# Performance work log

Measured on AMD Instinct MI355X. Metric: run time of the kernel, lower is better.

## Reference

```python
import jax, jax.numpy as jnp
import numpy as np

B, S, H, E, V = 64, 96, 1024, 512, 32000
START_TOKEN = 1


def setup_inputs() -> dict:
    key = jax.random.key(0)
    ks = jax.random.split(key, 12)
    sc = 0.02
    return {
        "encoder_outputs": jax.random.normal(ks[0], (B, S, H), jnp.float32),
        "encoder_hidden": jax.random.normal(ks[1], (1, B, H), jnp.float32),
        "emb_table": jax.random.normal(ks[2], (V, E), jnp.float32) * sc,
        "Wa": jax.random.normal(ks[3], (H, H), jnp.float32) * sc,
        "Ua": jax.random.normal(ks[4], (H, H), jnp.float32) * sc,
        "Va": jax.random.normal(ks[5], (H,), jnp.float32) * sc,
        "W_ih": jax.random.normal(ks[6], (3 * H, E + H), jnp.float32) * sc,
        "W_hh": jax.random.normal(ks[7], (3 * H, H), jnp.float32) * sc,
        "b_ih": jax.random.normal(ks[8], (3 * H,), jnp.float32) * sc,
        "b_hh": jax.random.normal(ks[9], (3 * H,), jnp.float32) * sc,
        "W_out": jax.random.normal(ks[10], (V, H), jnp.float32) * sc,
        "b_out": jax.random.normal(ks[11], (V,), jnp.float32) * sc,
        "max_length": 32,
    }


def _decode(encoder_outputs, encoder_hidden, emb_table, Wa, Ua, Va,
            W_ih, W_hh, b_ih, b_hh, W_out, b_out, max_length):
    keys = encoder_outputs                       # [B,S,H]
    keys_Ua = jnp.einsum('bsh,gh->bsg', keys, Ua)  # Ua(keys), hoisted (same math every step)
    h0 = encoder_hidden[0]                       # [B,H], num_layers==1
    tok0 = jnp.full((keys.shape[0],), START_TOKEN, dtype=jnp.int32)

    def step(carry, _):
        h, tok = carry
        emb = jax.nn.relu(emb_table[tok])                        # [B,E]
        # Bahdanau scores: Va(tanh(Wa(q)) + Ua(keys))  (tanh only on Wa(q), as in source)
        q = jnp.tanh(h @ Wa.T)                                   # [B,H]
        scores = jnp.einsum('bsh,h->bs', q[:, None, :] + keys_Ua, Va)  # [B,S]
        w = jax.nn.softmax(scores, axis=-1)                      # [B,S]
        ctx = jnp.einsum('bs,bsh->bh', w, keys)                  # [B,H]
        x = jnp.concatenate([emb, ctx], axis=-1)                 # [B,E+H]
        # GRU cell (torch gate order: r, z, n)
        gi = x @ W_ih.T + b_ih                                   # [B,3H]
        gh = h @ W_hh.T + b_hh
        Hd = h.shape[-1]
        r = jax.nn.sigmoid(gi[:, :Hd] + gh[:, :Hd])
        z = jax.nn.sigmoid(gi[:, Hd:2 * Hd] + gh[:, Hd:2 * Hd])
        n = jnp.tanh(gi[:, 2 * Hd:] + r * gh[:, 2 * Hd:])
        h_new = (1.0 - z) * n + z * h
        logits = h_new @ W_out.T + b_out                         # [B,V]
        tok_new = jnp.argmax(logits, axis=-1).astype(jnp.int32)  # greedy (no teacher forcing)
        return (h_new, tok_new), (logits, w)

    (h_T, _), (logits_seq, attn_seq) = jax.lax.scan(step, (h0, tok0), None, length=max_length)
    decoder_outputs = jnp.transpose(logits_seq, (1, 0, 2))  # [B,T,V]
    attentions = jnp.transpose(attn_seq, (1, 0, 2))         # [B,T,S]
    return decoder_outputs, h_T[None], attentions


def reference(encoder_outputs, encoder_hidden, emb_table, Wa, Ua, Va,
              W_ih, W_hh, b_ih, b_hh, W_out, b_out, max_length):
    return _decode(encoder_outputs, encoder_hidden, emb_table, Wa, Ua, Va,
                   W_ih, W_hh, b_ih, b_hh, W_out, b_out, max_length)
```

## Files before the change

kernel.cpp:

```cpp
#include <hip/hip_runtime.h>
#include <hip/hip_bf16.h>

#define Bdim 64
#define Sdim 96
#define Hdim 1024
#define Edim 512
#define Vdim 32000
#define Tdim 32
#define O1 65536000L
#define O2 65601536L
#define TV 1024000L

typedef short short8 __attribute__((ext_vector_type(8)));
typedef float f32x4 __attribute__((ext_vector_type(4)));

__device__ __forceinline__ unsigned short f2bf(float f) {
  unsigned u = __builtin_bit_cast(unsigned, f);
  unsigned r = (u + 0x7fffu + ((u >> 16) & 1u)) >> 16;
  return (unsigned short)r;
}


__global__ void k_u1(const float* __restrict__ Va, const float* __restrict__ Ua,
                     float* __restrict__ pu) {
  int gc = blockIdx.x & 15, hc = blockIdx.x >> 4;
  int lane = threadIdx.x & 63, wv = threadIdx.x >> 6;
  int g = gc * 64 + lane;
  int h0 = hc * 128 + wv * 32;
  float acc = 0.f;
  #pragma unroll 8
  for (int h = h0; h < h0 + 32; ++h) acc = fmaf(Va[h], Ua[(long)h * Hdim + g], acc);
  __shared__ float red[4][64];
  red[wv][lane] = acc;
  __syncthreads();
  if (threadIdx.x < 64)
    pu[hc * Hdim + gc * 64 + threadIdx.x] =
        red[0][threadIdx.x] + red[1][threadIdx.x] + red[2][threadIdx.x] + red[3][threadIdx.x];
}

__global__ void k_u2(const float* __restrict__ pu, float* __restrict__ u) {
  int g = blockIdx.x * 256 + threadIdx.x;
  float s = 0.f;
  #pragma unroll
  for (int i = 0; i < 8; ++i) s += pu[i * Hdim + g];
  u[g] = s;
}

__global__ void k_sc(const float* __restrict__ keys, const float* __restrict__ u,
                     float* __restrict__ sc) {
  int wid = blockIdx.x * 4 + (threadIdx.x >> 6);
  int lane = threadIdx.x & 63;
  int b = wid / Sdim, s = wid % Sdim;
  const float* kp = keys + ((long)b * Sdim + s) * Hdim;
  float acc = 0.f;
  #pragma unroll 4
  for (int g = lane; g < Hdim; g += 64) acc = fmaf(kp[g], u[g], acc);
  for (int off = 32; off; off >>= 1) acc += __shfl_down(acc, off);
  if (lane == 0) sc[wid] = acc;
}

__global__ void k_softmax(const float* __restrict__ sc, float* __restrict__ wbuf,
                          float* __restrict__ attn) {
  int b = blockIdx.x, tid = threadIdx.x;
  __shared__ float sv[128];
  __shared__ float sw[Sdim];
  float v = (tid < Sdim) ? sc[b * Sdim + tid] : -1e30f;
  sv[tid] = v;
  __syncthreads();
  for (int off = 64; off >= 1; off >>= 1) {
    if (tid < off) sv[tid] = fmaxf(sv[tid], sv[tid + off]);
    __syncthreads();
  }
  float mx = sv[0];
  __syncthreads();
  float e = (tid < Sdim) ? expf(v - mx) : 0.f;
  sv[tid] = e;
  __syncthreads();
  for (int off = 64; off >= 1; off >>= 1) {
    if (tid < off) sv[tid] += sv[tid + off];
    __syncthreads();
  }
  float sm = sv[0];
  if (tid < Sdim) {
    float w = e / sm;
    sw[tid] = w;
    wbuf[b * Sdim + tid] = w;
  }
  __syncthreads();
  for (int i = tid; i < Tdim * Sdim; i += 128)
    attn[(long)b * (Tdim * Sdim) + i] = sw[i % Sdim];
}

__global__ void k_ctx(const float* __restrict__ wbuf, const float* __restrict__ keys,
                      float* __restrict__ ctxT) {
  int b = blockIdx.x >> 3, slab = blockIdx.x & 7;
  int tid = threadIdx.x;
  __shared__ float sw[Sdim];
  __shared__ float4 red[8][32];
  if (tid < Sdim) sw[tid] = wbuf[b * Sdim + tid];
  __syncthreads();
  int hq = tid & 31, sg = tid >> 5;
  const float* kp = keys + ((long)b * Sdim + sg * 12) * Hdim + slab * 128 + hq * 4;
  float4 acc = {0.f, 0.f, 0.f, 0.f};
  #pragma unroll
  for (int s = 0; s < 12; ++s) {
    float4 k4 = *(const float4*)(kp + (long)s * Hdim);
    float w = sw[sg * 12 + s];
    acc.x = fmaf(w, k4.x, acc.x); acc.y = fmaf(w, k4.y, acc.y);
    acc.z = fmaf(w, k4.z, acc.z); acc.w = fmaf(w, k4.w, acc.w);
  }
  red[sg][hq] = acc;
  __syncthreads();
  if (tid < 128) {
    int hq2 = tid >> 2, c = tid & 3;
    float s = 0.f;
    #pragma unroll
    for (int i = 0; i < 8; ++i) s += ((const float*)&red[i][hq2])[c];
    ctxT[(slab * 128 + hq2 * 4 + c) * 64 + b] = s;
  }
}

__global__ void k_gctx(const float* __restrict__ ctxT, const float* __restrict__ Wih,
                       const float* __restrict__ bih, float* __restrict__ gctxT) {
  int j = blockIdx.x;
  int lane = threadIdx.x & 63, wv = threadIdx.x >> 6;
  const float* wp = Wih + (long)j * 1536 + Edim + wv * 256;
  const float* xp = ctxT + (wv * 256) * 64 + lane;
  float acc = 0.f;
  #pragma unroll 8
  for (int h = 0; h < 256; ++h) acc = fmaf(xp[h * 64], wp[h], acc);
  __shared__ float red[4][64];
  red[wv][lane] = acc;
  __syncthreads();
  if (threadIdx.x < 64)
    gctxT[(long)j * 64 + threadIdx.x] = red[0][threadIdx.x] + red[1][threadIdx.x] +
                                        red[2][threadIdx.x] + red[3][threadIdx.x] + bih[j];
}

__global__ void k_init(const float* __restrict__ h0, const float* __restrict__ embt,
                       float* __restrict__ hT, float* __restrict__ embT) {
  int idx = blockIdx.x * 256 + threadIdx.x;
  if (idx < Bdim * Hdim) {
    int b = idx >> 10, k = idx & 1023;
    hT[k * 64 + b] = h0[idx];
  } else {
    int j = idx - Bdim * Hdim;
    if (j < Edim * 64) {
      int e = j >> 6;
      float x = embt[1 * Edim + e];
      embT[j] = x > 0.f ? x : 0.f;
    }
  }
}

__global__ void k_w2b(const float* __restrict__ W, unsigned short* __restrict__ Wb) {
  long i = ((long)blockIdx.x * 256 + threadIdx.x) * 8;
  float4 a = *(const float4*)(W + i);
  float4 b = *(const float4*)(W + i + 4);
  short8 v;
  v[0] = (short)f2bf(a.x); v[1] = (short)f2bf(a.y); v[2] = (short)f2bf(a.z); v[3] = (short)f2bf(a.w);
  v[4] = (short)f2bf(b.x); v[5] = (short)f2bf(b.y); v[6] = (short)f2bf(b.z); v[7] = (short)f2bf(b.w);
  *(short8*)(Wb + i) = v;
}


__launch_bounds__(512)
__global__ void k_gru(const float* __restrict__ hT_in, float* __restrict__ hT_out,
                      const float* __restrict__ embT, const float* __restrict__ gctxT,
                      const float* __restrict__ Wih, const float* __restrict__ Whh,
                      const float* __restrict__ bhh,
                      float* __restrict__ hrow, unsigned short* __restrict__ hb) {
  __shared__ float wE[6][Edim];
  __shared__ float wH[6][Hdim];
  __shared__ float red[8][12][64];
  int tid = threadIdx.x, lane = tid & 63, wv = tid >> 6;
  int hid0 = blockIdx.x * 2;
  for (int i = tid; i < 6 * 128; i += 512) {
    int r = i >> 7, c = (i & 127) << 2;
    int row = (r >> 1) * Hdim + hid0 + (r & 1);
    *(float4*)&wE[r][c] = *(const float4*)(Wih + (long)row * 1536 + c);
  }
  for (int i = tid; i < 6 * 256; i += 512) {
    int r = i >> 8, c = (i & 255) << 2;
    int row = (r >> 1) * Hdim + hid0 + (r & 1);
    *(float4*)&wH[r][c] = *(const float4*)(Whh + (long)row * Hdim + c);
  }
  __syncthreads();
  float aE[6] = {0, 0, 0, 0, 0, 0}, aH[6] = {0, 0, 0, 0, 0, 0};
  int e0 = wv * 64;
  #pragma unroll 2
  for (int e = e0; e < e0 + 64; e += 4) {
    float x0 = embT[(e + 0) * 64 + lane];
    float x1 = embT[(e + 1) * 64 + lane];
    float x2 = embT[(e + 2) * 64 + lane];
    float x3 = embT[(e + 3) * 64 + lane];
    #pragma unroll
    for (int r = 0; r < 6; ++r) {
      float4 w = *(const float4*)&wE[r][e];
      aE[r] = fmaf(w.x, x0, aE[r]); aE[r] = fmaf(w.y, x1, aE[r]);
      aE[r] = fmaf(w.z, x2, aE[r]); aE[r] = fmaf(w.w, x3, aE[r]);
    }
  }
  int k0 = wv * 128;
  #pragma unroll 2
  for (int k = k0; k < k0 + 128; k += 4) {
    float x0 = hT_in[(k + 0) * 64 + lane];
    float x1 = hT_in[(k + 1) * 64 + lane];
    float x2 = hT_in[(k + 2) * 64 + lane];
    float x3 = hT_in[(k + 3) * 64 + lane];
    #pragma unroll
    for (int r = 0; r < 6; ++r) {
      float4 w = *(const float4*)&wH[r][k];
      aH[r] = fmaf(w.x, x0, aH[r]); aH[r] = fmaf(w.y, x1, aH[r]);
      aH[r] = fmaf(w.z, x2, aH[r]); aH[r] = fmaf(w.w, x3, aH[r]);
    }
  }
  #pragma unroll
  for (int r = 0; r < 6; ++r) {
    red[wv][r][lane] = aE[r];
    red[wv][6 + r][lane] = aH[r];
  }
  __syncthreads();
  if (tid < 128) {
    int hi = tid >> 6, b = tid & 63, hid = hid0 + hi;
    float sE[3] = {0, 0, 0}, sH[3] = {0, 0, 0};
    #pragma unroll
    for (int w2 = 0; w2 < 8; ++w2) {
      #pragma unroll
      for (int q = 0; q < 3; ++q) {
        sE[q] += red[w2][q * 2 + hi][b];
        sH[q] += red[w2][6 + q * 2 + hi][b];
      }
    }
    float gr = gctxT[(long)(0 * Hdim + hid) * 64 + b] + sE[0];
    float gz = gctxT[(long)(1 * Hdim + hid) * 64 + b] + sE[1];
    float gn = gctxT[(long)(2 * Hdim + hid) * 64 + b] + sE[2];
    float hr = sH[0] + bhh[hid];
    float hz = sH[1] + bhh[Hdim + hid];
    float hn = sH[2] + bhh[2 * Hdim + hid];
    float r = 1.f / (1.f + expf(-(gr + hr)));
    float z = 1.f / (1.f + expf(-(gz + hz)));
    float n = tanhf(gn + r * hn);
    float hold = hT_in[hid * 64 + b];
    float hnew = (1.f - z) * n + z * hold;
    hT_out[hid * 64 + b] = hnew;
    hrow[b * Hdim + hid] = hnew;
    hb[b * Hdim + hid] = f2bf(hnew);
  }
}

template <int WB>
__device__ __forceinline__ short8 loadB(const unsigned short* Bq, const float* Bqf, int off) {
  if (WB) {
    return *(const short8*)(Bq + off);
  } else {
    float4 x = *(const float4*)(Bqf + off);
    float4 y = *(const float4*)(Bqf + off + 4);
    short8 v;
    v[0] = (short)f2bf(x.x); v[1] = (short)f2bf(x.y); v[2] = (short)f2bf(x.z); v[3] = (short)f2bf(x.w);
    v[4] = (short)f2bf(y.x); v[5] = (short)f2bf(y.y); v[6] = (short)f2bf(y.z); v[7] = (short)f2bf(y.w);
    return v;
  }
}

template <int WB>
__launch_bounds__(256)
__global__ void k_logits(const unsigned short* __restrict__ hbv,
                         const unsigned short* __restrict__ Wb,
                         const float* __restrict__ Wf,
                         const float* __restrict__ bout, float* __restrict__ out,
                         int t, float* __restrict__ wsmax) {
  int tid = threadIdx.x, wv = tid >> 6, lane = tid & 63;
  int l15 = lane & 15, quad = lane >> 4;
  int n32 = (blockIdx.x * 4 + wv) * 32;
  int vcol0 = n32 + l15, vcol1 = n32 + 16 + l15;
  f32x4 acc[2][4];
  #pragma unroll
  for (int nt = 0; nt < 2; ++nt)
    #pragma unroll
    for (int mt = 0; mt < 4; ++mt) acc[nt][mt] = (f32x4){0.f, 0.f, 0.f, 0.f};
  const unsigned short* A = hbv + l15 * Hdim + quad * 8;
  const unsigned short* Bq0 = WB ? (Wb + (long)vcol0 * Hdim + quad * 8) : nullptr;
  const unsigned short* Bq1 = WB ? (Wb + (long)vcol1 * Hdim + quad * 8) : nullptr;
  const float* Bf0 = WB ? nullptr : (Wf + (long)vcol0 * Hdim + quad * 8);
  const float* Bf1 = WB ? nullptr : (Wf + (long)vcol1 * Hdim + quad * 8);
  short8 b0c = loadB<WB>(Bq0, Bf0, 0);
  short8 b1c = loadB<WB>(Bq1, Bf1, 0);
  #pragma unroll 4
  for (int ks = 0; ks < 32; ++ks) {
    int k0 = ks * 32;
    short8 b0n, b1n;
    if (ks < 31) {
      b0n = loadB<WB>(Bq0, Bf0, k0 + 32);
      b1n = loadB<WB>(Bq1, Bf1, k0 + 32);
    }
    short8 a0 = *(const short8*)(A + k0);
    short8 a1 = *(const short8*)(A + 16 * Hdim + k0);
    short8 a2 = *(const short8*)(A + 32 * Hdim + k0);
    short8 a3 = *(const short8*)(A + 48 * Hdim + k0);
    acc[0][0] = __builtin_amdgcn_mfma_f32_16x16x32_bf16(a0, b0c, acc[0][0], 0, 0, 0);
    acc[0][1] = __builtin_amdgcn_mfma_f32_16x16x32_bf16(a1, b0c, acc[0][1], 0, 0, 0);
    acc[0][2] = __builtin_amdgcn_mfma_f32_16x16x32_bf16(a2, b0c, acc[0][2], 0, 0, 0);
    acc[0][3] = __builtin_amdgcn_mfma_f32_16x16x32_bf16(a3, b0c, acc[0][3], 0, 0, 0);
    acc[1][0] = __builtin_amdgcn_mfma_f32_16x16x32_bf16(a0, b1c, acc[1][0], 0, 0, 0);
    acc[1][1] = __builtin_amdgcn_mfma_f32_16x16x32_bf16(a1, b1c, acc[1][1], 0, 0, 0);
    acc[1][2] = __builtin_amdgcn_mfma_f32_16x16x32_bf16(a2, b1c, acc[1][2], 0, 0, 0);
    acc[1][3] = __builtin_amdgcn_mfma_f32_16x16x32_bf16(a3, b1c, acc[1][3], 0, 0, 0);
    b0c = b0n; b1c = b1n;
  }
  __shared__ float lmax[4][64];
  float bo0 = bout[vcol0], bo1 = bout[vcol1];
  float* Ot = out + (long)t * Vdim;
  #pragma unroll
  for (int mt = 0; mt < 4; ++mt) {
    #pragma unroll
    for (int r = 0; r < 4; ++r) {
      int brow = mt * 16 + quad * 4 + r;
      float v0 = acc[0][mt][r] + bo0;
      float v1 = acc[1][mt][r] + bo1;
      Ot[(long)brow * TV + vcol0] = v0;
      Ot[(long)brow * TV + vcol1] = v1;
      float m = fmaxf(v0, v1);
      m = fmaxf(m, __shfl_xor(m, 1));
      m = fmaxf(m, __shfl_xor(m, 2));
      m = fmaxf(m, __shfl_xor(m, 4));
      m = fmaxf(m, __shfl_xor(m, 8));
      if (l15 == 0) lmax[wv][brow] = m;
    }
  }
  __syncthreads();
  if (tid < 64) {
    float m = fmaxf(fmaxf(lmax[0][tid], lmax[1][tid]), fmaxf(lmax[2][tid], lmax[3][tid]));
    wsmax[tid * 256 + blockIdx.x] = m;
  }
}

__global__ void k_argmax(const float* __restrict__ wsmax, const float* __restrict__ out,
                         const float* __restrict__ hrow, const float* __restrict__ Wout,
                         const float* __restrict__ bout, const float* __restrict__ embt,
                         float* __restrict__ embT, int t) {
  int b = blockIdx.x, tid = threadIdx.x;
  __shared__ float lred[4];
  __shared__ float thr_s;
  __shared__ int qn, cnt, tok_s;
  __shared__ int qblk[32];
  __shared__ int cand[64];
  __shared__ float cval[64];
  float mv = (tid < 250) ? wsmax[b * 256 + tid] : -1e30f;
  float m = mv;
  for (int off = 32; off; off >>= 1) m = fmaxf(m, __shfl_down(m, off));
  if ((tid & 63) == 0) lred[tid >> 6] = m;
  if (tid == 0) { qn = 0; cnt = 0; }
  __syncthreads();
  if (tid == 0)
    thr_s = fmaxf(fmaxf(lred[0], lred[1]), fmaxf(lred[2], lred[3])) - 0.03f;
  __syncthreads();
  float thr = thr_s;
  if (mv >= thr) {
    int i = atomicAdd(&qn, 1);
    if (i < 32) qblk[i] = tid;
  }
  __syncthreads();
  int QN = min(qn, 32);
  const float* L = out + (long)b * TV + (long)t * Vdim;
  for (int j = tid; j < QN * 128; j += 256) {
    int blk = qblk[j >> 7];
    int v = blk * 128 + (j & 127);
    float val = L[v];
    if (val >= thr) {
      int i = atomicAdd(&cnt, 1);
      if (i < 64) cand[i] = v;
    }
  }
  __syncthreads();
  int C = min(cnt, 64);
  int tok;
  if (C == 1) {
    tok = cand[0];
  } else {
    for (int c = 0; c < C; ++c) {
      int v = cand[c];
      const float* wr = Wout + (long)v * Hdim;
      const float* hr = hrow + b * Hdim;
      float p = 0.f;
      for (int k = tid; k < Hdim; k += 256) p = fmaf(hr[k], wr[k], p);
      for (int off = 32; off; off >>= 1) p += __shfl_down(p, off);
      __syncthreads();
      if ((tid & 63) == 0) lred[tid >> 6] = p;
      __syncthreads();
      if (tid == 0) cval[c] = lred[0] + lred[1] + lred[2] + lred[3] + bout[v];
    }
    __syncthreads();
    if (tid == 0) {
      float best = -1e30f;
      int bi = 0x7fffffff;
      for (int c = 0; c < C; ++c)
        if (cval[c] > best || (cval[c] == best && cand[c] < bi)) { best = cval[c]; bi = cand[c]; }
      tok_s = bi;
    }
    __syncthreads();
    tok = tok_s;
  }
  for (int e = tid; e < Edim; e += 256) {
    float x = embt[(long)tok * Edim + e];
    embT[e * 64 + b] = x > 0.f ? x : 0.f;
  }
}


extern "C" void kernel_launch(void* const* d_in, const int* in_sizes, int n_in,
                              void* d_out, int out_size, void* d_ws, size_t ws_size,
                              hipStream_t stream) {
  const float* keys = (const float*)d_in[0];
  const float* h0   = (const float*)d_in[1];
  const float* embt = (const float*)d_in[2];
  const float* Ua   = (const float*)d_in[4];
  const float* Va   = (const float*)d_in[5];
  const float* Wih  = (const float*)d_in[6];
  const float* Whh  = (const float*)d_in[7];
  const float* bih  = (const float*)d_in[8];
  const float* bhh  = (const float*)d_in[9];
  const float* Wout = (const float*)d_in[10];
  const float* bout = (const float*)d_in[11];
  float* out = (float*)d_out;

  char* ws = (char*)d_ws;
  float* u     = (float*)(ws + 0);
  float* pu    = (float*)(ws + 4096);
  float* sc    = (float*)(ws + 36864);
  float* wbuf  = (float*)(ws + 61440);
  float* ctxT  = (float*)(ws + 86016);
  float* gctxT = (float*)(ws + 348160);
  float* hTa   = (float*)(ws + 1134592);
  float* hTb   = (float*)(ws + 1396736);
  float* embT  = (float*)(ws + 1658880);
  float* wsmax = (float*)(ws + 1789952);
  unsigned short* hb = (unsigned short*)(ws + 1855488);
  unsigned short* Wb = (unsigned short*)(ws + 1986560);
  bool useBf = ws_size >= 67522560ull;

  float* houtrow = out + O1;
  float* attn = out + O2;

  k_u1<<<128, 256, 0, stream>>>(Va, Ua, pu);
  k_u2<<<4, 256, 0, stream>>>(pu, u);
  k_sc<<<1536, 256, 0, stream>>>(keys, u, sc);
  k_softmax<<<64, 128, 0, stream>>>(sc, wbuf, attn);
  k_ctx<<<512, 256, 0, stream>>>(wbuf, keys, ctxT);
  k_gctx<<<3072, 256, 0, stream>>>(ctxT, Wih, bih, gctxT);
  k_init<<<384, 256, 0, stream>>>(h0, embt, hTa, embT);
  if (useBf) k_w2b<<<16000, 256, 0, stream>>>(Wout, Wb);

  float* hin = hTa;
  float* hout = hTb;
  for (int t = 0; t < Tdim; ++t) {
    k_gru<<<512, 512, 0, stream>>>(hin, hout, embT, gctxT, Wih, Whh, bhh, houtrow, hb);
    if (useBf)
      k_logits<1><<<250, 256, 0, stream>>>(hb, Wb, nullptr, bout, out, t, wsmax);
    else
      k_logits<0><<<250, 256, 0, stream>>>(hb, nullptr, Wout, bout, out, t, wsmax);
    if (t < Tdim - 1)
      k_argmax<<<64, 256, 0, stream>>>(wsmax, out, houtrow, Wout, bout, embt, embT, t);
    float* tmp = hin; hin = hout; hout = tmp;
  }
}
```

Baseline: 3.683 ms.

## Fuse per-step GRU, logits and argmax into one persistent cooperative kernel

Replaces the 3-kernels-per-step decode loop with a single cooperative kernel of 256 blocks that loops over all timesteps, using grid.sync between the GRU, logits and argmax phases. The aim is to remove roughly 95 kernel launches and their launch gaps. The GRU phase now reads weights straight from global memory instead of staging them in LDS, with each block covering 4 hidden units. The logits phase uses one 16-column tile per wave. Running only 256 blocks and paying grid-wide barriers may cut parallelism for the GRU and logits phases.

```diff
diff --git a/kernel.cpp b/kernel.cpp
--- a/kernel.cpp
+++ b/kernel.cpp
@@ -1,5 +1,8 @@
 #include <hip/hip_runtime.h>
 #include <hip/hip_bf16.h>
+#include <hip/hip_cooperative_groups.h>
+
+namespace cg = cooperative_groups;
 
 #define Bdim 64
 #define Sdim 96
@@ -163,92 +166,6 @@
   *(short8*)(Wb + i) = v;
 }
 
-
-__launch_bounds__(512)
-__global__ void k_gru(const float* __restrict__ hT_in, float* __restrict__ hT_out,
-                      const float* __restrict__ embT, const float* __restrict__ gctxT,
-                      const float* __restrict__ Wih, const float* __restrict__ Whh,
-                      const float* __restrict__ bhh,
-                      float* __restrict__ hrow, unsigned short* __restrict__ hb) {
-  __shared__ float wE[6][Edim];
-  __shared__ float wH[6][Hdim];
-  __shared__ float red[8][12][64];
-  int tid = threadIdx.x, lane = tid & 63, wv = tid >> 6;
-  int hid0 = blockIdx.x * 2;
-  for (int i = tid; i < 6 * 128; i += 512) {
-    int r = i >> 7, c = (i & 127) << 2;
-    int row = (r >> 1) * Hdim + hid0 + (r & 1);
-    *(float4*)&wE[r][c] = *(const float4*)(Wih + (long)row * 1536 + c);
-  }
-  for (int i = tid; i < 6 * 256; i += 512) {
-    int r = i >> 8, c = (i & 255) << 2;
-    int row = (r >> 1) * Hdim + hid0 + (r & 1);
-    *(float4*)&wH[r][c] = *(const float4*)(Whh + (long)row * Hdim + c);
-  }
-  __syncthreads();
-  float aE[6] = {0, 0, 0, 0, 0, 0}, aH[6] = {0, 0, 0, 0, 0, 0};
-  int e0 = wv * 64;
-  #pragma unroll 2
-  for (int e = e0; e < e0 + 64; e += 4) {
-    float x0 = embT[(e + 0) * 64 + lane];
-    float x1 = embT[(e + 1) * 64 + lane];
-    float x2 = embT[(e + 2) * 64 + lane];
-    float x3 = embT[(e + 3) * 64 + lane];
-    #pragma unroll
-    for (int r = 0; r < 6; ++r) {
-      float4 w = *(const float4*)&wE[r][e];
-      aE[r] = fmaf(w.x, x0, aE[r]); aE[r] = fmaf(w.y, x1, aE[r]);
-      aE[r] = fmaf(w.z, x2, aE[r]); aE[r] = fmaf(w.w, x3, aE[r]);
-    }
-  }
-  int k0 = wv * 128;
-  #pragma unroll 2
-  for (int k = k0; k < k0 + 128; k += 4) {
-    float x0 = hT_in[(k + 0) * 64 + lane];
-    float x1 = hT_in[(k + 1) * 64 + lane];
-    float x2 = hT_in[(k + 2) * 64 + lane];
-    float x3 = hT_in[(k + 3) * 64 + lane];
-    #pragma unroll
-    for (int r = 0; r < 6; ++r) {
-      float4 w = *(const float4*)&wH[r][k];
-      aH[r] = fmaf(w.x, x0, aH[r]); aH[r] = fmaf(w.y, x1, aH[r]);
-      aH[r] = fmaf(w.z, x2, aH[r]); aH[r] = fmaf(w.w, x3, aH[r]);
-    }
-  }
-  #pragma unroll
-  for (int r = 0; r < 6; ++r) {
-    red[wv][r][lane] = aE[r];
-    red[wv][6 + r][lane] = aH[r];
-  }
-  __syncthreads();
-  if (tid < 128) {
-    int hi = tid >> 6, b = tid & 63, hid = hid0 + hi;
-    float sE[3] = {0, 0, 0}, sH[3] = {0, 0, 0};
-    #pragma unroll
-    for (int w2 = 0; w2 < 8; ++w2) {
-      #pragma unroll
-      for (int q = 0; q < 3; ++q) {
-        sE[q] += red[w2][q * 2 + hi][b];
-        sH[q] += red[w2][6 + q * 2 + hi][b];
-      }
-    }
-    float gr = gctxT[(long)(0 * Hdim + hid) * 64 + b] + sE[0];
-    float gz = gctxT[(long)(1 * Hdim + hid) * 64 + b] + sE[1];
-    float gn = gctxT[(long)(2 * Hdim + hid) * 64 + b] + sE[2];
-    float hr = sH[0] + bhh[hid];
-    float hz = sH[1] + bhh[Hdim + hid];
-    float hn = sH[2] + bhh[2 * Hdim + hid];
-    float r = 1.f / (1.f + expf(-(gr + hr)));
-    float z = 1.f / (1.f + expf(-(gz + hz)));
-    float n = tanhf(gn + r * hn);
-    float hold = hT_in[hid * 64 + b];
-    float hnew = (1.f - z) * n + z * hold;
-    hT_out[hid * 64 + b] = hnew;
-    hrow[b * Hdim + hid] = hnew;
-    hb[b * Hdim + hid] = f2bf(hnew);
-  }
-}
-
 template <int WB>
 __device__ __forceinline__ short8 loadB(const unsigned short* Bq, const float* Bqf, int off) {
   if (WB) {
@@ -264,146 +181,239 @@
 }
 
 template <int WB>
-__launch_bounds__(256)
-__global__ void k_logits(const unsigned short* __restrict__ hbv,
+__launch_bounds__(512, 2)
+__global__ void k_decode(unsigned short* __restrict__ hb,
                          const unsigned short* __restrict__ Wb,
-                         const float* __restrict__ Wf,
-                         const float* __restrict__ bout, float* __restrict__ out,
-                         int t, float* __restrict__ wsmax) {
-  int tid = threadIdx.x, wv = tid >> 6, lane = tid & 63;
-  int l15 = lane & 15, quad = lane >> 4;
-  int n32 = (blockIdx.x * 4 + wv) * 32;
-  int vcol0 = n32 + l15, vcol1 = n32 + 16 + l15;
-  f32x4 acc[2][4];
-  #pragma unroll
-  for (int nt = 0; nt < 2; ++nt)
-    #pragma unroll
-    for (int mt = 0; mt < 4; ++mt) acc[nt][mt] = (f32x4){0.f, 0.f, 0.f, 0.f};
-  const unsigned short* A = hbv + l15 * Hdim + quad * 8;
-  const unsigned short* Bq0 = WB ? (Wb + (long)vcol0 * Hdim + quad * 8) : nullptr;
-  const unsigned short* Bq1 = WB ? (Wb + (long)vcol1 * Hdim + quad * 8) : nullptr;
-  const float* Bf0 = WB ? nullptr : (Wf + (long)vcol0 * Hdim + quad * 8);
-  const float* Bf1 = WB ? nullptr : (Wf + (long)vcol1 * Hdim + quad * 8);
-  short8 b0c = loadB<WB>(Bq0, Bf0, 0);
-  short8 b1c = loadB<WB>(Bq1, Bf1, 0);
-  #pragma unroll 4
-  for (int ks = 0; ks < 32; ++ks) {
-    int k0 = ks * 32;
-    short8 b0n, b1n;
-    if (ks < 31) {
-      b0n = loadB<WB>(Bq0, Bf0, k0 + 32);
-      b1n = loadB<WB>(Bq1, Bf1, k0 + 32);
-    }
-    short8 a0 = *(const short8*)(A + k0);
-    short8 a1 = *(const short8*)(A + 16 * Hdim + k0);
-    short8 a2 = *(const short8*)(A + 32 * Hdim + k0);
-    short8 a3 = *(const short8*)(A + 48 * Hdim + k0);
-    acc[0][0] = __builtin_amdgcn_mfma_f32_16x16x32_bf16(a0, b0c, acc[0][0], 0, 0, 0);
-    acc[0][1] = __builtin_amdgcn_mfma_f32_16x16x32_bf16(a1, b0c, acc[0][1], 0, 0, 0);
-    acc[0][2] = __builtin_amdgcn_mfma_f32_16x16x32_bf16(a2, b0c, acc[0][2], 0, 0, 0);
-    acc[0][3] = __builtin_amdgcn_mfma_f32_16x16x32_bf16(a3, b0c, acc[0][3], 0, 0, 0);
-    acc[1][0] = __builtin_amdgcn_mfma_f32_16x16x32_bf16(a0, b1c, acc[1][0], 0, 0, 0);
-    acc[1][1] = __builtin_amdgcn_mfma_f32_16x16x32_bf16(a1, b1c, acc[1][1], 0, 0, 0);
-    acc[1][2] = __builtin_amdgcn_mfma_f32_16x16x32_bf16(a2, b1c, acc[1][2], 0, 0, 0);
-    acc[1][3] = __builtin_amdgcn_mfma_f32_16x16x32_bf16(a3, b1c, acc[1][3], 0, 0, 0);
-    b0c = b0n; b1c = b1n;
-  }
-  __shared__ float lmax[4][64];
-  float bo0 = bout[vcol0], bo1 = bout[vcol1];
-  float* Ot = out + (long)t * Vdim;
-  #pragma unroll
-  for (int mt = 0; mt < 4; ++mt) {
-    #pragma unroll
-    for (int r = 0; r < 4; ++r) {
-      int brow = mt * 16 + quad * 4 + r;
-      float v0 = acc[0][mt][r] + bo0;
-      float v1 = acc[1][mt][r] + bo1;
-      Ot[(long)brow * TV + vcol0] = v0;
-      Ot[(long)brow * TV + vcol1] = v1;
-      float m = fmaxf(v0, v1);
-      m = fmaxf(m, __shfl_xor(m, 1));
-      m = fmaxf(m, __shfl_xor(m, 2));
-      m = fmaxf(m, __shfl_xor(m, 4));
-      m = fmaxf(m, __shfl_xor(m, 8));
-      if (l15 == 0) lmax[wv][brow] = m;
-    }
-  }
-  __syncthreads();
-  if (tid < 64) {
-    float m = fmaxf(fmaxf(lmax[0][tid], lmax[1][tid]), fmaxf(lmax[2][tid], lmax[3][tid]));
-    wsmax[tid * 256 + blockIdx.x] = m;
-  }
-}
-
-__global__ void k_argmax(const float* __restrict__ wsmax, const float* __restrict__ out,
-                         const float* __restrict__ hrow, const float* __restrict__ Wout,
-                         const float* __restrict__ bout, const float* __restrict__ embt,
-                         float* __restrict__ embT, int t) {
-  int b = blockIdx.x, tid = threadIdx.x;
-  __shared__ float lred[4];
+                         const float* __restrict__ Wout,
+                         const float* __restrict__ bout,
+                         float* __restrict__ out,
+                         float* __restrict__ hTa, float* __restrict__ hTb,
+                         float* __restrict__ embT,
+                         const float* __restrict__ gctxT,
+                         const float* __restrict__ Wih,
+                         const float* __restrict__ Whh,
+                         const float* __restrict__ bhh,
+                         float* __restrict__ hrow,
+                         float* __restrict__ wsmax,
+                         const float* __restrict__ embt) {
+  cg::grid_group grid = cg::this_grid();
+  __shared__ float red[8][24][64];
+  __shared__ float lmax[8][64];
+  __shared__ float lred[8];
   __shared__ float thr_s;
   __shared__ int qn, cnt, tok_s;
   __shared__ int qblk[32];
   __shared__ int cand[64];
   __shared__ float cval[64];
-  float mv = (tid < 250) ? wsmax[b * 256 + tid] : -1e30f;
-  float m = mv;
-  for (int off = 32; off; off >>= 1) m = fmaxf(m, __shfl_down(m, off));
-  if ((tid & 63) == 0) lred[tid >> 6] = m;
-  if (tid == 0) { qn = 0; cnt = 0; }
-  __syncthreads();
-  if (tid == 0)
-    thr_s = fmaxf(fmaxf(lred[0], lred[1]), fmaxf(lred[2], lred[3])) - 0.03f;
-  __syncthreads();
-  float thr = thr_s;
-  if (mv >= thr) {
-    int i = atomicAdd(&qn, 1);
-    if (i < 32) qblk[i] = tid;
-  }
-  __syncthreads();
-  int QN = min(qn, 32);
-  const float* L = out + (long)b * TV + (long)t * Vdim;
-  for (int j = tid; j < QN * 128; j += 256) {
-    int blk = qblk[j >> 7];
-    int v = blk * 128 + (j & 127);
-    float val = L[v];
-    if (val >= thr) {
-      int i = atomicAdd(&cnt, 1);
-      if (i < 64) cand[i] = v;
+
+  const int tid = threadIdx.x, lane = tid & 63, wv = tid >> 6;
+  const int bid = blockIdx.x;
+
+  #pragma unroll 1
+  for (int t = 0; t < Tdim; ++t) {
+    const float* hin = (t & 1) ? hTb : hTa;
+    float* hout = (t & 1) ? hTa : hTb;
+
+    {
+      const int hid0 = bid * 4;
+      float acc[12];
+      #pragma unroll
+      for (int r = 0; r < 12; ++r) acc[r] = 0.f;
+      {
+        const int e0 = wv * 64;
+        for (int e = e0; e < e0 + 64; e += 4) {
+          float x0 = embT[(e + 0) * 64 + lane];
+          float x1 = embT[(e + 1) * 64 + lane];
+          float x2 = embT[(e + 2) * 64 + lane];
+          float x3 = embT[(e + 3) * 64 + lane];
+          #pragma unroll
+          for (int r = 0; r < 12; ++r) {
+            int row = (r >> 2) * Hdim + hid0 + (r & 3);
+            float4 w = *(const float4*)(Wih + (long)row * 1536 + e);
+            acc[r] = fmaf(w.x, x0, acc[r]); acc[r] = fmaf(w.y, x1, acc[r]);
+            acc[r] = fmaf(w.z, x2, acc[r]); acc[r] = fmaf(w.w, x3, acc[r]);
+          }
+        }
+        #pragma unroll
+        for (int r = 0; r < 12; ++r) red[wv][r][lane] = acc[r];
+      }
+      #pragma unroll
+      for (int r = 0; r < 12; ++r) acc[r] = 0.f;
+      {
+        const int k0 = wv * 128;
+        for (int k = k0; k < k0 + 128; k += 4) {
+          float x0 = hin[(k + 0) * 64 + lane];
+          float x1 = hin[(k + 1) * 64 + lane];
+          float x2 = hin[(k + 2) * 64 + lane];
+          float x3 = hin[(k + 3) * 64 + lane];
+          #pragma unroll
+          for (int r = 0; r < 12; ++r) {
+            int row = (r >> 2) * Hdim + hid0 + (r & 3);
+            float4 w = *(const float4*)(Whh + (long)row * Hdim + k);
+            acc[r] = fmaf(w.x, x0, acc[r]); acc[r] = fmaf(w.y, x1, acc[r]);
+            acc[r] = fmaf(w.z, x2, acc[r]); acc[r] = fmaf(w.w, x3, acc[r]);
+          }
+        }
+        #pragma unroll
+        for (int r = 0; r < 12; ++r) red[wv][12 + r][lane] = acc[r];
+      }
+      __syncthreads();
+      if (tid < 256) {
+        int hh = tid >> 6, b = tid & 63, hid = hid0 + hh;
+        float sE0 = 0.f, sE1 = 0.f, sE2 = 0.f, sH0 = 0.f, sH1 = 0.f, sH2 = 0.f;
+        #pragma unroll
+        for (int w2 = 0; w2 < 8; ++w2) {
+          sE0 += red[w2][0 + hh][b];
+          sE1 += red[w2][4 + hh][b];
+          sE2 += red[w2][8 + hh][b];
+          sH0 += red[w2][12 + hh][b];
+          sH1 += red[w2][16 + hh][b];
+          sH2 += red[w2][20 + hh][b];
+        }
+        float gr = gctxT[(long)(0 * Hdim + hid) * 64 + b] + sE0;
+        float gz = gctxT[(long)(1 * Hdim + hid) * 64 + b] + sE1;
+        float gn = gctxT[(long)(2 * Hdim + hid) * 64 + b] + sE2;
+        float hr = sH0 + bhh[hid];
+        float hz = sH1 + bhh[Hdim + hid];
+        float hn = sH2 + bhh[2 * Hdim + hid];
+        float rr = 1.f / (1.f + expf(-(gr + hr)));
+        float zz = 1.f / (1.f + expf(-(gz + hz)));
+        float nn = tanhf(gn + rr * hn);
+        float hold = hin[hid * 64 + b];
+        float hnew = (1.f - zz) * nn + zz * hold;
+        hout[hid * 64 + b] = hnew;
+        hrow[b * Hdim + hid] = hnew;
+        hb[b * Hdim + hid] = f2bf(hnew);
+      }
     }
-  }
-  __syncthreads();
-  int C = min(cnt, 64);
-  int tok;
-  if (C == 1) {
-    tok = cand[0];
-  } else {
-    for (int c = 0; c < C; ++c) {
-      int v = cand[c];
-      const float* wr = Wout + (long)v * Hdim;
-      const float* hr = hrow + b * Hdim;
-      float p = 0.f;
-      for (int k = tid; k < Hdim; k += 256) p = fmaf(hr[k], wr[k], p);
-      for (int off = 32; off; off >>= 1) p += __shfl_down(p, off);
+    grid.sync();
+
+    if (bid < 250) {
+      int l15 = lane & 15, quad = lane >> 4;
+      int vcol = bid * 128 + wv * 16 + l15;
+      f32x4 acc4[4];
+      #pragma unroll
+      for (int mt = 0; mt < 4; ++mt) acc4[mt] = (f32x4){0.f, 0.f, 0.f, 0.f};
+      const unsigned short* A = hb + l15 * Hdim + quad * 8;
+      const unsigned short* Bq = WB ? (Wb + (long)vcol * Hdim + quad * 8) : nullptr;
+      const float* Bf = WB ? nullptr : (Wout + (long)vcol * Hdim + quad * 8);
+      short8 bc = loadB<WB>(Bq, Bf, 0);
+      #pragma unroll 4
+      for (int ks = 0; ks < 32; ++ks) {
+        int k0 = ks * 32;
+        short8 bn;
+        if (ks < 31) bn = loadB<WB>(Bq, Bf, k0 + 32);
+        short8 a0 = *(const short8*)(A + k0);
+        short8 a1 = *(const short8*)(A + 16 * Hdim + k0);
+        short8 a2 = *(const short8*)(A + 32 * Hdim + k0);
+        short8 a3 = *(const short8*)(A + 48 * Hdim + k0);
+        acc4[0] = __builtin_amdgcn_mfma_f32_16x16x32_bf16(a0, bc, acc4[0], 0, 0, 0);
+        acc4[1] = __builtin_amdgcn_mfma_f32_16x16x32_bf16(a1, bc, acc4[1], 0, 0, 0);
+        acc4[2] = __builtin_amdgcn_mfma_f32_16x16x32_bf16(a2, bc, acc4[2], 0, 0, 0);
+        acc4[3] = __builtin_amdgcn_mfma_f32_16x16x32_bf16(a3, bc, acc4[3], 0, 0, 0);
+        bc = bn;
+      }
+      float bo = bout[vcol];
+      float* Ot = out + (long)t * Vdim;
+      #pragma unroll
+      for (int mt = 0; mt < 4; ++mt) {
+        #pragma unroll
+        for (int r = 0; r < 4; ++r) {
+          int brow = mt * 16 + quad * 4 + r;
+          float v = acc4[mt][r] + bo;
+          Ot[(long)brow * TV + vcol] = v;
+          float m = v;
+          m = fmaxf(m, __shfl_xor(m, 1));
+          m = fmaxf(m, __shfl_xor(m, 2));
+          m = fmaxf(m, __shfl_xor(m, 4));
+          m = fmaxf(m, __shfl_xor(m, 8));
+          if (l15 == 0) lmax[wv][brow] = m;
+        }
+      }
       __syncthreads();
-      if ((tid & 63) == 0) lred[tid >> 6] = p;
-      __syncthreads();
-      if (tid == 0) cval[c] = lred[0] + lred[1] + lred[2] + lred[3] + bout[v];
+      if (tid < 64) {
+        float m = lmax[0][tid];
+        #pragma unroll
+        for (int w2 = 1; w2 < 8; ++w2) m = fmaxf(m, lmax[w2][tid]);
+        wsmax[tid * 256 + bid] = m;
+      }
     }
-    __syncthreads();
-    if (tid == 0) {
-      float best = -1e30f;
-      int bi = 0x7fffffff;
-      for (int c = 0; c < C; ++c)
-        if (cval[c] > best || (cval[c] == best && cand[c] < bi)) { best = cval[c]; bi = cand[c]; }
-      tok_s = bi;
+    grid.sync();
+
+    if (t < Tdim - 1) {
+      if (bid < 64) {
+        int b = bid;
+        float mv = (tid < 250) ? wsmax[b * 256 + tid] : -1e30f;
+        float m = mv;
+        for (int off = 32; off; off >>= 1) m = fmaxf(m, __shfl_down(m, off));
+        if (lane == 0) lred[wv] = m;
+        if (tid == 0) { qn = 0; cnt = 0; }
+        __syncthreads();
+        if (tid == 0) {
+          float mm = lred[0];
+          #pragma unroll
+          for (int i = 1; i < 8; ++i) mm = fmaxf(mm, lred[i]);
+          thr_s = mm - 0.03f;
+        }
+        __syncthreads();
+        float thr = thr_s;
+        if (mv >= thr) {
+          int i = atomicAdd(&qn, 1);
+          if (i < 32) qblk[i] = tid;
+        }
+        __syncthreads();
+        int QN = min(qn, 32);
+        const float* L = out + (long)b * TV + (long)t * Vdim;
+        for (int j = tid; j < QN * 128; j += 512) {
+          int blk = qblk[j >> 7];
+          int v = blk * 128 + (j & 127);
+          float val = L[v];
+          if (val >= thr) {
+            int i = atomicAdd(&cnt, 1);
+            if (i < 64) cand[i] = v;
+          }
+        }
+        __syncthreads();
+        int C = min(cnt, 64);
+        int tok;
+        if (C == 1) {
+          tok = cand[0];
+        } else {
+          for (int c = 0; c < C; ++c) {
+            int v = cand[c];
+            const float* wr = Wout + (long)v * Hdim;
+            const float* hp = hrow + b * Hdim;
+            float p = 0.f;
+            #pragma unroll
+            for (int k = tid; k < Hdim; k += 512) p = fmaf(hp[k], wr[k], p);
+            for (int off = 32; off; off >>= 1) p += __shfl_down(p, off);
+            if (lane == 0) lred[wv] = p;
+            __syncthreads();
+            if (tid == 0) {
+              float s = 0.f;
+              #pragma unroll
+              for (int i = 0; i < 8; ++i) s += lred[i];
+              cval[c] = s + bout[v];
+            }
+            __syncthreads();
+          }
+          if (tid == 0) {
+            float best = -1e30f;
+            int bi = 0x7fffffff;
+            for (int c = 0; c < C; ++c)
+              if (cval[c] > best || (cval[c] == best && cand[c] < bi)) { best = cval[c]; bi = cand[c]; }
+            tok_s = bi;
+          }
+          __syncthreads();
+          tok = tok_s;
+        }
+        {
+          float x = embt[(long)tok * Edim + tid];
+          embT[tid * 64 + b] = x > 0.f ? x : 0.f;
+        }
+      }
+      grid.sync();
     }
-    __syncthreads();
-    tok = tok_s;
-  }
-  for (int e = tid; e < Edim; e += 256) {
-    float x = embt[(long)tok * Edim + e];
-    embT[e * 64 + b] = x > 0.f ? x : 0.f;
   }
 }
 
@@ -451,16 +461,11 @@
   k_init<<<384, 256, 0, stream>>>(h0, embt, hTa, embT);
   if (useBf) k_w2b<<<16000, 256, 0, stream>>>(Wout, Wb);
 
-  float* hin = hTa;
-  float* hout = hTb;
-  for (int t = 0; t < Tdim; ++t) {
-    k_gru<<<512, 512, 0, stream>>>(hin, hout, embT, gctxT, Wih, Whh, bhh, houtrow, hb);
-    if (useBf)
-      k_logits<1><<<250, 256, 0, stream>>>(hb, Wb, nullptr, bout, out, t, wsmax);
-    else
-      k_logits<0><<<250, 256, 0, stream>>>(hb, nullptr, Wout, bout, out, t, wsmax);
-    if (t < Tdim - 1)
-      k_argmax<<<64, 256, 0, stream>>>(wsmax, out, houtrow, Wout, bout, embt, embT, t);
-    float* tmp = hin; hin = hout; hout = tmp;
-  }
-}
+  void* kargs[] = {(void*)&hb,    (void*)&Wb,    (void*)&Wout, (void*)&bout,
+                   (void*)&out,   (void*)&hTa,   (void*)&hTb,  (void*)&embT,
+                   (void*)&gctxT, (void*)&Wih,   (void*)&Whh,  (void*)&bhh,
+                   (void*)&houtrow, (void*)&wsmax, (void*)&embt};
+  const void* fn = useBf ? reinterpret_cast<const void*>(&k_decode<1>)
+                         : reinterpret_cast<const void*>(&k_decode<0>);
+  hipLaunchCooperativeKernel(fn, dim3(256), dim3(512), kargs, 0, stream);
+}
```

Result: slower. 6.632 ms (+80.1%).
